# Optimization experiments

Hardware: AMD Instinct MI355X
Metric: run time of the kernel (lower is better)

The kernel has to match this reference:

```python
import jax, jax.numpy as jnp
import numpy as np

N = 50000   # nodes
E = 800000  # edges
D = 128     # input_dim == hidden_dim
R = 8       # num_relations
B = 2       # num_blocks


def setup_inputs() -> dict:
    key = jax.random.key(0)
    ks = jax.random.split(key, 9)
    x = jax.random.normal(ks[0], (N, D), dtype=jnp.float32)
    edge_index = jax.random.randint(ks[1], (2, E), 0, N, dtype=jnp.int32)
    edge_type = jax.random.randint(ks[2], (E,), 0, R, dtype=jnp.int32)
    s_blk = 1.0 / np.sqrt(D // B)
    s_root = 1.0 / np.sqrt(D)
    W1 = jax.random.normal(ks[3], (R, B, D // B, D // B), dtype=jnp.float32) * s_blk
    root1 = jax.random.normal(ks[4], (D, D), dtype=jnp.float32) * s_root
    b1 = jnp.zeros((D,), dtype=jnp.float32)
    W2 = jax.random.normal(ks[5], (R, B, D // B, D // B), dtype=jnp.float32) * s_blk
    root2 = jax.random.normal(ks[6], (D, D), dtype=jnp.float32) * s_root
    b2 = jnp.zeros((D,), dtype=jnp.float32)
    return {"x": x, "edge_index": edge_index, "edge_type": edge_type,
            "W1": W1, "root1": root1, "b1": b1,
            "W2": W2, "root2": root2, "b2": b2}


def rgcn_conv(x, src, dst, etype, W, root, bias):
    # PyG RGCNConv (num_blocks mode): per-relation MEAN aggregation of source
    # features, block-diagonal transform, summed over relations, plus root + bias.
    # Transform is linear, so aggregate first (saves per-edge matmuls).
    n = x.shape[0]
    r, b, ib, ob = W.shape
    xs = x[src]                                   # [E, d_in] gather
    seg = dst * r + etype                          # fused (node, relation) id
    sums = jax.ops.segment_sum(xs, seg, num_segments=n * r)        # [n*r, d_in]
    cnt = jax.ops.segment_sum(jnp.ones((xs.shape[0],), xs.dtype), seg,
                              num_segments=n * r)                   # [n*r]
    mean = sums / jnp.maximum(cnt, 1.0)[:, None]   # zero where no edges
    agg = mean.reshape(n, r, b, ib)                # [n, R, blocks, in/blocks]
    out = jnp.einsum('nrbc,rbcd->nbd', agg, W).reshape(n, b * ob)
    return out + x @ root + bias


def reference(x, edge_index, edge_type, W1, root1, b1, W2, root2, b2):
    src, dst = edge_index[0], edge_index[1]
    h = jax.nn.relu(rgcn_conv(x, src, dst, edge_type, W1, root1, b1))
    # dropout(p=0.2) is identity in eval mode (reference uses eval semantics)
    return rgcn_conv(h, src, dst, edge_type, W2, root2, b2)
```

## Files before the change

### kernel.cpp

```cpp
#include <hip/hip_runtime.h>

#define NN 50000
#define EE 800000
#define DD 128
#define RR 8
#define CELLS (NN * RR)
#define TILE_N 64
#define NBLK ((NN + TILE_N - 1) / TILE_N)
#define SCAN_CHUNK 1024
#define SCAN_BLOCKS ((CELLS + SCAN_CHUNK - 1) / SCAN_CHUNK)

typedef __attribute__((ext_vector_type(4))) float f32x4;
typedef __attribute__((ext_vector_type(8))) short s16x8;
union ABu { uint4 q; s16x8 v; };


__device__ __forceinline__ unsigned int packbf2(float a, float b) {
    unsigned int ua = __float_as_uint(a);
    unsigned int ub = __float_as_uint(b);
    ua = (ua + 0x7fffu + ((ua >> 16) & 1u)) >> 16;
    ub = (ub + 0x7fffu + ((ub >> 16) & 1u)) & 0xffff0000u;
    return ua | ub;
}

__device__ __forceinline__ void upadd16(float* sA, uint4 a, uint4 b) {
    unsigned int u[8] = {a.x, a.y, a.z, a.w, b.x, b.y, b.z, b.w};
#pragma unroll
    for (int j = 0; j < 8; ++j) {
        sA[2 * j]     += __uint_as_float(u[j] << 16);
        sA[2 * j + 1] += __uint_as_float(u[j] & 0xffff0000u);
    }
}

#define NB_A ((NN * 32 + 255) / 256)
#define NB_B 128
#define NB_C 32
#define NB_D ((EE + 255) / 256)

__global__ void prep_fused(const float* __restrict__ x, unsigned int* __restrict__ xb,
                           const float* __restrict__ W1, const float* __restrict__ W2,
                           unsigned int* __restrict__ Wb1, unsigned int* __restrict__ Wb2,
                           const float* __restrict__ r1, const float* __restrict__ r2,
                           unsigned int* __restrict__ rb1, unsigned int* __restrict__ rb2,
                           const int* __restrict__ dst, const int* __restrict__ et,
                           int* __restrict__ cnt) {
    int bid = blockIdx.x, tid = threadIdx.x;
    if (bid < NB_A) {
        int i = bid * 256 + tid;
        if (i < NN * 32) {
            float4 v = ((const float4*)x)[i];
            ((uint2*)xb)[i] = make_uint2(packbf2(v.x, v.y), packbf2(v.z, v.w));
        }
    } else if (bid < NB_A + NB_B) {
        int i = (bid - NB_A) * 256 + tid;
        int kp = i & 31, n = (i >> 5) & 63, rb = i >> 11;
        int s0 = (rb * 64 + 2 * kp) * 64 + n;
        int s1 = (rb * 64 + 2 * kp + 1) * 64 + n;
        Wb1[((rb * 64 + n) * 32) + kp] = packbf2(W1[s0], W1[s1]);
        Wb2[((rb * 64 + n) * 32) + kp] = packbf2(W2[s0], W2[s1]);
    } else if (bid < NB_A + NB_B + NB_C) {
        int i = (bid - NB_A - NB_B) * 256 + tid;
        int kp = i & 63, n = i >> 6;
        int s0 = (2 * kp) * 128 + n, s1 = (2 * kp + 1) * 128 + n;
        rb1[n * 64 + kp] = packbf2(r1[s0], r1[s1]);
        rb2[n * 64 + kp] = packbf2(r2[s0], r2[s1]);
    } else {
        int e = (bid - NB_A - NB_B - NB_C) * 256 + tid;
        if (e < EE) atomicAdd(&cnt[et[e] * NN + dst[e]], 1);
    }
}


__global__ __launch_bounds__(256) void scan1(const int* __restrict__ cnt,
                                             int* __restrict__ off, int* __restrict__ bsum) {
    __shared__ int s[256];
    int tid = threadIdx.x;
    int base = blockIdx.x * SCAN_CHUNK + tid * 4;
    int v[4];
#pragma unroll
    for (int i = 0; i < 4; ++i) v[i] = (base + i < CELLS) ? cnt[base + i] : 0;
    int tot = v[0] + v[1] + v[2] + v[3];
    s[tid] = tot;
    __syncthreads();
    for (int d = 1; d < 256; d <<= 1) {
        int t = (tid >= d) ? s[tid - d] : 0;
        __syncthreads();
        s[tid] += t;
        __syncthreads();
    }
    int excl = s[tid] - tot;
    if (tid == 255) bsum[blockIdx.x] = s[255];
    int run = excl;
#pragma unroll
    for (int i = 0; i < 4; ++i) {
        if (base + i < CELLS) off[base + i] = run;
        run += v[i];
    }
}

__global__ __launch_bounds__(256) void scan3(int* __restrict__ off, const int* __restrict__ bsum,
                                             int* __restrict__ cur) {
    __shared__ int red[256];
    int tid = threadIdx.x, bid = blockIdx.x;
    int a = 0;
    for (int i = tid; i < bid; i += 256) a += bsum[i];
    red[tid] = a;
    __syncthreads();
#pragma unroll
    for (int d = 128; d > 0; d >>= 1) {
        if (tid < d) red[tid] += red[tid + d];
        __syncthreads();
    }
    int add = red[0];
    int base = bid * SCAN_CHUNK + tid * 4;
#pragma unroll
    for (int i = 0; i < 4; ++i) {
        int c = base + i;
        if (c < CELLS) {
            int o = off[c] + add;
            off[c] = o;
            cur[c] = o;
        }
    }
    if (bid == 0 && tid == 0) off[CELLS] = EE;
}

__global__ void cell_scatter(const int* __restrict__ src, const int* __restrict__ dst,
                             const int* __restrict__ et, int* __restrict__ cur,
                             int* __restrict__ esrc) {
    int e = blockIdx.x * blockDim.x + threadIdx.x;
    if (e < EE) {
        int cell = et[e] * NN + dst[e];
        int pos = atomicAdd(&cur[cell], 1);
        esrc[pos] = src[e];
    }
}

template <int RELU, int WRITEF, int WRITEB>
__global__ __launch_bounds__(512, 4) void layer_fused(
    const unsigned int* __restrict__ xgb, const int* __restrict__ esrc,
    const int* __restrict__ off,
    const unsigned int* __restrict__ Wb, const unsigned int* __restrict__ rootb,
    const float* __restrict__ bias, float* __restrict__ outf,
    unsigned int* __restrict__ outb) {

    __shared__ unsigned int SH[8320];
    unsigned int* MT = SH;

    int tid = threadIdx.x;
    int n0 = blockIdx.x * TILE_N;
    int e = tid & 63, q = tid >> 6;
    int w = tid >> 6, l = tid & 63;
    int quad = l >> 4, li = l & 15;
    int b = w >> 2;

    f32x4 acc[4];
    {
        float bb = bias[16 * w + li];
#pragma unroll
        for (int mt = 0; mt < 4; ++mt) {
            acc[mt][0] = bb; acc[mt][1] = bb; acc[mt][2] = bb; acc[mt][3] = bb;
        }
    }

    int node = n0 + e;

    for (int r = 0; r < RR; ++r) {
        float sA[16];
#pragma unroll
        for (int i = 0; i < 16; ++i) sA[i] = 0.f;
        int ne = 0;
        if (node < NN) {
            int cell = r * NN + node;
            int o = off[cell];
            ne = off[cell + 1] - o;
            int t2 = 0;
            for (; t2 + 2 <= ne; t2 += 2) {
                int s0 = esrc[o + t2], s1 = esrc[o + t2 + 1];
                const uint4* p0 = (const uint4*)(xgb + (size_t)s0 * 64 + q * 8);
                const uint4* p1 = (const uint4*)(xgb + (size_t)s1 * 64 + q * 8);
                uint4 A0 = p0[0], A1 = p0[1];
                uint4 B0 = p1[0], B1 = p1[1];
                upadd16(sA, A0, A1);
                upadd16(sA, B0, B1);
            }
            if (t2 < ne) {
                int s0 = esrc[o + t2];
                const uint4* p0 = (const uint4*)(xgb + (size_t)s0 * 64 + q * 8);
                uint4 A0 = p0[0], A1 = p0[1];
                upadd16(sA, A0, A1);
            }
        }
        float sc = 1.0f / (float)max(ne, 1);

        __syncthreads();
#pragma unroll
        for (int i = 0; i < 8; ++i)
            MT[(8 * q + i) * 67 + e] = packbf2(sA[2 * i] * sc, sA[2 * i + 1] * sc);
        __syncthreads();

        const uint4* WbB = (const uint4*)(Wb + (((size_t)r * 2 + b) * 64) * 32);
        int nloc = (w & 3) * 16 + li;
#pragma unroll
        for (int kc = 0; kc < 2; ++kc) {
            ABu bf;
            bf.q = WbB[nloc * 8 + 4 * kc + quad];
#pragma unroll
            for (int mt = 0; mt < 4; ++mt) {
                ABu af;
                int base = (32 * b + 16 * kc + 4 * quad) * 67 + 16 * mt + li;
                af.q.x = MT[base]; af.q.y = MT[base + 67];
                af.q.z = MT[base + 134]; af.q.w = MT[base + 201];
                acc[mt] = __builtin_amdgcn_mfma_f32_16x16x32_bf16(af.v, bf.v, acc[mt], 0, 0, 0);
            }
        }
    }
    __syncthreads();

    if (node < NN) {
        const uint4* xr = (const uint4*)(xgb + (size_t)node * 64 + q * 8);
        uint4 X0 = xr[0], X1 = xr[1];
        MT[(8 * q + 0) * 67 + e] = X0.x;
        MT[(8 * q + 1) * 67 + e] = X0.y;
        MT[(8 * q + 2) * 67 + e] = X0.z;
        MT[(8 * q + 3) * 67 + e] = X0.w;
        MT[(8 * q + 4) * 67 + e] = X1.x;
        MT[(8 * q + 5) * 67 + e] = X1.y;
        MT[(8 * q + 6) * 67 + e] = X1.z;
        MT[(8 * q + 7) * 67 + e] = X1.w;
    } else {
#pragma unroll
        for (int i = 0; i < 8; ++i) MT[(8 * q + i) * 67 + e] = 0u;
    }
    __syncthreads();

    const uint4* RbB = (const uint4*)rootb;
#pragma unroll
    for (int kc = 0; kc < 4; ++kc) {
        ABu bf;
        bf.q = RbB[(16 * w + li) * 16 + 4 * kc + quad];
#pragma unroll
        for (int mt = 0; mt < 4; ++mt) {
            ABu af;
            int base = (16 * kc + 4 * quad) * 67 + 16 * mt + li;
            af.q.x = MT[base]; af.q.y = MT[base + 67];
            af.q.z = MT[base + 134]; af.q.w = MT[base + 201];
            acc[mt] = __builtin_amdgcn_mfma_f32_16x16x32_bf16(af.v, bf.v, acc[mt], 0, 0, 0);
        }
    }
    __syncthreads();

    float* OF = (float*)SH;
#pragma unroll
    for (int mt = 0; mt < 4; ++mt)
#pragma unroll
        for (int reg = 0; reg < 4; ++reg)
            OF[(16 * mt + 4 * quad + reg) * 130 + 16 * w + li] = acc[mt][reg];
    __syncthreads();

    if (WRITEB) {
        int p = tid & 63, rg = tid >> 6;
#pragma unroll 4
        for (int it = 0; it < 8; ++it) {
            int ee = it * 8 + rg, row = n0 + ee;
            if (row < NN) {
                float v0 = OF[ee * 130 + 2 * p], v1 = OF[ee * 130 + 2 * p + 1];
                if (RELU) { v0 = fmaxf(v0, 0.f); v1 = fmaxf(v1, 0.f); }
                outb[(size_t)row * 64 + p] = packbf2(v0, v1);
            }
        }
    }
    if (WRITEF) {
        int d4 = (tid & 31) * 4, rg = tid >> 5;
#pragma unroll 4
        for (int it = 0; it < 4; ++it) {
            int ee = it * 16 + rg, row = n0 + ee;
            if (row < NN) {
                float4 v = make_float4(OF[ee * 130 + d4], OF[ee * 130 + d4 + 1],
                                       OF[ee * 130 + d4 + 2], OF[ee * 130 + d4 + 3]);
                if (RELU) {
                    v.x = fmaxf(v.x, 0.f); v.y = fmaxf(v.y, 0.f);
                    v.z = fmaxf(v.z, 0.f); v.w = fmaxf(v.w, 0.f);
                }
                *(float4*)(outf + (size_t)row * DD + d4) = v;
            }
        }
    }
}


extern "C" void kernel_launch(void* const* d_in, const int* in_sizes, int n_in,
                              void* d_out, int out_size, void* d_ws, size_t ws_size,
                              hipStream_t stream) {
    const float* x     = (const float*)d_in[0];
    const int*   ei    = (const int*)d_in[1];
    const int*   src   = ei;
    const int*   dstp  = ei + EE;
    const int*   et    = (const int*)d_in[2];
    const float* W1    = (const float*)d_in[3];
    const float* root1 = (const float*)d_in[4];
    const float* b1    = (const float*)d_in[5];
    const float* W2    = (const float*)d_in[6];
    const float* root2 = (const float*)d_in[7];
    const float* b2    = (const float*)d_in[8];
    float* out = (float*)d_out;

    unsigned int* xb  = (unsigned int*)d_ws;
    unsigned int* hb  = xb + (size_t)NN * 64;
    int* cnt  = (int*)(hb + (size_t)NN * 64);
    int* off  = cnt + CELLS;
    int* cur  = off + CELLS + 1;
    int* bsum = cur + CELLS;
    int* esrc = bsum + 512;
    unsigned int* Wb1 = (unsigned int*)(esrc + EE);
    unsigned int* Wb2 = Wb1 + 32768;
    unsigned int* rb1 = Wb2 + 32768;
    unsigned int* rb2 = rb1 + 8192;

    hipMemsetAsync(cnt, 0, CELLS * sizeof(int), stream);
    prep_fused<<<NB_A + NB_B + NB_C + NB_D, 256, 0, stream>>>(
        x, xb, W1, W2, Wb1, Wb2, root1, root2, rb1, rb2, dstp, et, cnt);
    scan1<<<SCAN_BLOCKS, 256, 0, stream>>>(cnt, off, bsum);
    scan3<<<SCAN_BLOCKS, 256, 0, stream>>>(off, bsum, cur);
    cell_scatter<<<(EE + 255) / 256, 256, 0, stream>>>(src, dstp, et, cur, esrc);

    layer_fused<1, 0, 1><<<NBLK, 512, 0, stream>>>(xb, esrc, off, Wb1, rb1, b1,
                                                   nullptr, hb);
    layer_fused<0, 1, 0><<<NBLK, 512, 0, stream>>>(hb, esrc, off, Wb2, rb2, b2,
                                                   out, nullptr);
}
```

Baseline: 366.5 us.

## Double-buffer relation tiles and overlap gathers with previous relation's MFMA

The layer kernel now preloads all per-relation offsets, issues the first four edge gathers for relation r before running the MFMA for relation r-1, and writes the aggregated means into alternating shared-memory buffers. This allows one barrier per relation instead of two. The goal is to hide gather latency behind matrix work and cut synchronisation. The prep kernel also remaps its weight-packing indices so reads from the source weights are coalesced. In exchange, register pressure rises from the prefetched uint4s and LDS use grows slightly, which may affect occupancy.

```diff
diff --git a/kernel.cpp b/kernel.cpp
--- a/kernel.cpp
+++ b/kernel.cpp
@@ -53,14 +53,14 @@
         }
     } else if (bid < NB_A + NB_B) {
         int i = (bid - NB_A) * 256 + tid;
-        int kp = i & 31, n = (i >> 5) & 63, rb = i >> 11;
+        int n = i & 63, kp = (i >> 6) & 31, rb = i >> 11;
         int s0 = (rb * 64 + 2 * kp) * 64 + n;
         int s1 = (rb * 64 + 2 * kp + 1) * 64 + n;
         Wb1[((rb * 64 + n) * 32) + kp] = packbf2(W1[s0], W1[s1]);
         Wb2[((rb * 64 + n) * 32) + kp] = packbf2(W2[s0], W2[s1]);
     } else if (bid < NB_A + NB_B + NB_C) {
         int i = (bid - NB_A - NB_B) * 256 + tid;
-        int kp = i & 63, n = i >> 6;
+        int n = i & 127, kp = i >> 7;
         int s0 = (2 * kp) * 128 + n, s1 = (2 * kp + 1) * 128 + n;
         rb1[n * 64 + kp] = packbf2(r1[s0], r1[s1]);
         rb2[n * 64 + kp] = packbf2(r2[s0], r2[s1]);
@@ -136,6 +136,8 @@
     }
 }
 
+#define MTSZ 4288
+
 template <int RELU, int WRITEF, int WRITEB>
 __global__ __launch_bounds__(512, 4) void layer_fused(
     const unsigned int* __restrict__ xgb, const int* __restrict__ esrc,
@@ -144,15 +146,15 @@
     const float* __restrict__ bias, float* __restrict__ outf,
     unsigned int* __restrict__ outb) {
 
-    __shared__ unsigned int SH[8320];
-    unsigned int* MT = SH;
+    __shared__ unsigned int SH[2 * MTSZ];
 
     int tid = threadIdx.x;
     int n0 = blockIdx.x * TILE_N;
     int e = tid & 63, q = tid >> 6;
-    int w = tid >> 6, l = tid & 63;
+    int w = q, l = e;
     int quad = l >> 4, li = l & 15;
     int b = w >> 2;
+    int nloc = (w & 3) * 16 + li;
 
     f32x4 acc[4];
     {
@@ -165,72 +167,93 @@
 
     int node = n0 + e;
 
+    int ov[RR], nv[RR];
+#pragma unroll
     for (int r = 0; r < RR; ++r) {
+        if (node < NN) {
+            int c = r * NN + node;
+            int o = off[c];
+            ov[r] = o;
+            nv[r] = off[c + 1] - o;
+        } else { ov[r] = 0; nv[r] = 0; }
+    }
+
+#define MFMA_BLOCK(MTbase, rr) do {                                                   \
+    const uint4* WbB = (const uint4*)(Wb + (((size_t)(rr) * 2 + b) * 64) * 32);       \
+    _Pragma("unroll") for (int kc = 0; kc < 2; ++kc) {                                \
+        ABu bf; bf.q = WbB[nloc * 8 + 4 * kc + quad];                                 \
+        _Pragma("unroll") for (int mt = 0; mt < 4; ++mt) {                            \
+            ABu af; int base_ = (32 * b + 16 * kc + 4 * quad) * 67 + 16 * mt + li;    \
+            af.q.x = (MTbase)[base_];       af.q.y = (MTbase)[base_ + 67];            \
+            af.q.z = (MTbase)[base_ + 134]; af.q.w = (MTbase)[base_ + 201];           \
+            acc[mt] = __builtin_amdgcn_mfma_f32_16x16x32_bf16(af.v, bf.v, acc[mt], 0, 0, 0); \
+        } } } while (0)
+
+#pragma unroll
+    for (int r = 0; r < RR; ++r) {
+        int ne = nv[r], o = ov[r];
+        int s0 = 0, s1 = 0, s2 = 0, s3 = 0;
+        uint4 A0, B0, A1, B1, A2, B2, A3, B3;
+        if (ne > 0) s0 = esrc[o];
+        if (ne > 1) s1 = esrc[o + 1];
+        if (ne > 2) s2 = esrc[o + 2];
+        if (ne > 3) s3 = esrc[o + 3];
+        if (ne > 0) { const uint4* p = (const uint4*)(xgb + (size_t)s0 * 64 + q * 8); A0 = p[0]; B0 = p[1]; }
+        if (ne > 1) { const uint4* p = (const uint4*)(xgb + (size_t)s1 * 64 + q * 8); A1 = p[0]; B1 = p[1]; }
+        if (ne > 2) { const uint4* p = (const uint4*)(xgb + (size_t)s2 * 64 + q * 8); A2 = p[0]; B2 = p[1]; }
+        if (ne > 3) { const uint4* p = (const uint4*)(xgb + (size_t)s3 * 64 + q * 8); A3 = p[0]; B3 = p[1]; }
+
+        if (r > 0) MFMA_BLOCK(SH + ((r - 1) & 1) * MTSZ, r - 1);
+
         float sA[16];
 #pragma unroll
         for (int i = 0; i < 16; ++i) sA[i] = 0.f;
-        int ne = 0;
-        if (node < NN) {
-            int cell = r * NN + node;
-            int o = off[cell];
-            ne = off[cell + 1] - o;
-            int t2 = 0;
+        if (ne > 0) upadd16(sA, A0, B0);
+        if (ne > 1) upadd16(sA, A1, B1);
+        if (ne > 2) upadd16(sA, A2, B2);
+        if (ne > 3) upadd16(sA, A3, B3);
+        if (ne > 4) {
+            int t2 = 4;
             for (; t2 + 2 <= ne; t2 += 2) {
-                int s0 = esrc[o + t2], s1 = esrc[o + t2 + 1];
-                const uint4* p0 = (const uint4*)(xgb + (size_t)s0 * 64 + q * 8);
-                const uint4* p1 = (const uint4*)(xgb + (size_t)s1 * 64 + q * 8);
-                uint4 A0 = p0[0], A1 = p0[1];
-                uint4 B0 = p1[0], B1 = p1[1];
-                upadd16(sA, A0, A1);
-                upadd16(sA, B0, B1);
+                int u0 = esrc[o + t2], u1 = esrc[o + t2 + 1];
+                const uint4* p0 = (const uint4*)(xgb + (size_t)u0 * 64 + q * 8);
+                const uint4* p1 = (const uint4*)(xgb + (size_t)u1 * 64 + q * 8);
+                uint4 X0 = p0[0], X1 = p0[1];
+                uint4 Y0 = p1[0], Y1 = p1[1];
+                upadd16(sA, X0, X1);
+                upadd16(sA, Y0, Y1);
             }
             if (t2 < ne) {
-                int s0 = esrc[o + t2];
-                const uint4* p0 = (const uint4*)(xgb + (size_t)s0 * 64 + q * 8);
-                uint4 A0 = p0[0], A1 = p0[1];
-                upadd16(sA, A0, A1);
+                int u0 = esrc[o + t2];
+                const uint4* p0 = (const uint4*)(xgb + (size_t)u0 * 64 + q * 8);
+                uint4 X0 = p0[0], X1 = p0[1];
+                upadd16(sA, X0, X1);
             }
         }
         float sc = 1.0f / (float)max(ne, 1);
-
+        unsigned int* MTW = SH + (r & 1) * MTSZ;
+#pragma unroll
+        for (int i = 0; i < 8; ++i)
+            MTW[(8 * q + i) * 67 + e] = packbf2(sA[2 * i] * sc, sA[2 * i + 1] * sc);
         __syncthreads();
-#pragma unroll
-        for (int i = 0; i < 8; ++i)
-            MT[(8 * q + i) * 67 + e] = packbf2(sA[2 * i] * sc, sA[2 * i + 1] * sc);
-        __syncthreads();
-
-        const uint4* WbB = (const uint4*)(Wb + (((size_t)r * 2 + b) * 64) * 32);
-        int nloc = (w & 3) * 16 + li;
-#pragma unroll
-        for (int kc = 0; kc < 2; ++kc) {
-            ABu bf;
-            bf.q = WbB[nloc * 8 + 4 * kc + quad];
-#pragma unroll
-            for (int mt = 0; mt < 4; ++mt) {
-                ABu af;
-                int base = (32 * b + 16 * kc + 4 * quad) * 67 + 16 * mt + li;
-                af.q.x = MT[base]; af.q.y = MT[base + 67];
-                af.q.z = MT[base + 134]; af.q.w = MT[base + 201];
-                acc[mt] = __builtin_amdgcn_mfma_f32_16x16x32_bf16(af.v, bf.v, acc[mt], 0, 0, 0);
-            }
-        }
-    }
-    __syncthreads();
+    }
+
+    MFMA_BLOCK(SH + MTSZ, RR - 1);
 
     if (node < NN) {
         const uint4* xr = (const uint4*)(xgb + (size_t)node * 64 + q * 8);
         uint4 X0 = xr[0], X1 = xr[1];
-        MT[(8 * q + 0) * 67 + e] = X0.x;
-        MT[(8 * q + 1) * 67 + e] = X0.y;
-        MT[(8 * q + 2) * 67 + e] = X0.z;
-        MT[(8 * q + 3) * 67 + e] = X0.w;
-        MT[(8 * q + 4) * 67 + e] = X1.x;
-        MT[(8 * q + 5) * 67 + e] = X1.y;
-        MT[(8 * q + 6) * 67 + e] = X1.z;
-        MT[(8 * q + 7) * 67 + e] = X1.w;
+        SH[(8 * q + 0) * 67 + e] = X0.x;
+        SH[(8 * q + 1) * 67 + e] = X0.y;
+        SH[(8 * q + 2) * 67 + e] = X0.z;
+        SH[(8 * q + 3) * 67 + e] = X0.w;
+        SH[(8 * q + 4) * 67 + e] = X1.x;
+        SH[(8 * q + 5) * 67 + e] = X1.y;
+        SH[(8 * q + 6) * 67 + e] = X1.z;
+        SH[(8 * q + 7) * 67 + e] = X1.w;
     } else {
 #pragma unroll
-        for (int i = 0; i < 8; ++i) MT[(8 * q + i) * 67 + e] = 0u;
+        for (int i = 0; i < 8; ++i) SH[(8 * q + i) * 67 + e] = 0u;
     }
     __syncthreads();
 
@@ -243,8 +266,8 @@
         for (int mt = 0; mt < 4; ++mt) {
             ABu af;
             int base = (16 * kc + 4 * quad) * 67 + 16 * mt + li;
-            af.q.x = MT[base]; af.q.y = MT[base + 67];
-            af.q.z = MT[base + 134]; af.q.w = MT[base + 201];
+            af.q.x = SH[base]; af.q.y = SH[base + 67];
+            af.q.z = SH[base + 134]; af.q.w = SH[base + 201];
             acc[mt] = __builtin_amdgcn_mfma_f32_16x16x32_bf16(af.v, bf.v, acc[mt], 0, 0, 0);
         }
     }
@@ -286,6 +309,7 @@
             }
         }
     }
+#undef MFMA_BLOCK
 }
 
 
```

Measured after the change: 402.6 us. 9.8% more time.

## Aggregate neighbor features via one-hot MFMA over coalesced per-tile edge chunks

Applied to the files above, without the earlier changes.

Replaces the per-node serial gather-and-accumulate loop with a tile-level scheme. For each relation, the tile's contiguous edge range is processed in 64-edge chunks: rows are gathered coalesced into LDS, a one-hot selection matrix (built from the destination index packed into the low 6 bits of esrc) is written, and the segment sum is done with bf16 MFMA. This targets the load imbalance and poor coalescing of per-thread edge loops. In exchange it adds LDS use, extra syncs per chunk, and rounding of the one-hot product to bf16. It also relies on src<<6 fitting in 32 bits. The prep kernel's weight-packing loops are reindexed so global reads coalesce.

```diff
diff --git a/kernel.cpp b/kernel.cpp
--- a/kernel.cpp
+++ b/kernel.cpp
@@ -21,15 +21,6 @@
     ua = (ua + 0x7fffu + ((ua >> 16) & 1u)) >> 16;
     ub = (ub + 0x7fffu + ((ub >> 16) & 1u)) & 0xffff0000u;
     return ua | ub;
-}
-
-__device__ __forceinline__ void upadd16(float* sA, uint4 a, uint4 b) {
-    unsigned int u[8] = {a.x, a.y, a.z, a.w, b.x, b.y, b.z, b.w};
-#pragma unroll
-    for (int j = 0; j < 8; ++j) {
-        sA[2 * j]     += __uint_as_float(u[j] << 16);
-        sA[2 * j + 1] += __uint_as_float(u[j] & 0xffff0000u);
-    }
 }
 
 #define NB_A ((NN * 32 + 255) / 256)
@@ -53,14 +44,14 @@
         }
     } else if (bid < NB_A + NB_B) {
         int i = (bid - NB_A) * 256 + tid;
-        int kp = i & 31, n = (i >> 5) & 63, rb = i >> 11;
+        int n = i & 63, kp = (i >> 6) & 31, rb = i >> 11;
         int s0 = (rb * 64 + 2 * kp) * 64 + n;
         int s1 = (rb * 64 + 2 * kp + 1) * 64 + n;
         Wb1[((rb * 64 + n) * 32) + kp] = packbf2(W1[s0], W1[s1]);
         Wb2[((rb * 64 + n) * 32) + kp] = packbf2(W2[s0], W2[s1]);
     } else if (bid < NB_A + NB_B + NB_C) {
         int i = (bid - NB_A - NB_B) * 256 + tid;
-        int kp = i & 63, n = i >> 6;
+        int n = i & 127, kp = i >> 7;
         int s0 = (2 * kp) * 128 + n, s1 = (2 * kp + 1) * 128 + n;
         rb1[n * 64 + kp] = packbf2(r1[s0], r1[s1]);
         rb2[n * 64 + kp] = packbf2(r2[s0], r2[s1]);
@@ -130,29 +121,34 @@
                              int* __restrict__ esrc) {
     int e = blockIdx.x * blockDim.x + threadIdx.x;
     if (e < EE) {
-        int cell = et[e] * NN + dst[e];
+        int d = dst[e];
+        int cell = et[e] * NN + d;
         int pos = atomicAdd(&cur[cell], 1);
-        esrc[pos] = src[e];
+        esrc[pos] = (int)(((unsigned int)src[e] << 6) | (unsigned int)(d & 63));
     }
 }
 
 template <int RELU, int WRITEF, int WRITEB>
 __global__ __launch_bounds__(512, 4) void layer_fused(
-    const unsigned int* __restrict__ xgb, const int* __restrict__ esrc,
+    const unsigned int* __restrict__ xgb, const unsigned int* __restrict__ epk,
     const int* __restrict__ off,
     const unsigned int* __restrict__ Wb, const unsigned int* __restrict__ rootb,
     const float* __restrict__ bias, float* __restrict__ outf,
     unsigned int* __restrict__ outb) {
 
-    __shared__ unsigned int SH[8320];
-    unsigned int* MT = SH;
+    __shared__ __align__(16) unsigned int SH[11136];
+    unsigned int* GB  = SH;
+    unsigned int* SS  = SH + 4224;
+    unsigned int* MTp = SH + 6336;
+    float*        CF  = (float*)(SH + 10624);
 
     int tid = threadIdx.x;
     int n0 = blockIdx.x * TILE_N;
-    int e = tid & 63, q = tid >> 6;
     int w = tid >> 6, l = tid & 63;
     int quad = l >> 4, li = l & 15;
     int b = w >> 2;
+    int nloc = (w & 3) * 16 + li;
+    int node = n0 + l;
 
     f32x4 acc[4];
     {
@@ -163,44 +159,105 @@
         }
     }
 
-    int node = n0 + e;
+    int rng = 0;
+    {
+        int nend = n0 + TILE_N; if (nend > NN) nend = NN;
+        if (l < 8)       rng = off[l * NN + n0];
+        else if (l < 16) rng = off[(l - 8) * NN + nend];
+    }
+
+    uint4 z4 = make_uint4(0u, 0u, 0u, 0u);
+    ((uint4*)GB)[tid] = z4;
+    ((uint4*)GB)[512 + tid] = z4;
+    if (tid < 32) ((uint4*)GB)[1024 + tid] = z4;
+
+    if (w == 0) {
+        for (int r = 0; r < RR; ++r) {
+            float sc = 1.0f;
+            if (node < NN) {
+                int c = r * NN + node;
+                int ct = off[c + 1] - off[c];
+                sc = 1.0f / (float)max(ct, 1);
+            }
+            CF[r * 64 + l] = sc;
+        }
+    }
+    __syncthreads();
 
     for (int r = 0; r < RR; ++r) {
-        float sA[16];
-#pragma unroll
-        for (int i = 0; i < 16; ++i) sA[i] = 0.f;
-        int ne = 0;
-        if (node < NN) {
-            int cell = r * NN + node;
-            int o = off[cell];
-            ne = off[cell + 1] - o;
-            int t2 = 0;
-            for (; t2 + 2 <= ne; t2 += 2) {
-                int s0 = esrc[o + t2], s1 = esrc[o + t2 + 1];
-                const uint4* p0 = (const uint4*)(xgb + (size_t)s0 * 64 + q * 8);
-                const uint4* p1 = (const uint4*)(xgb + (size_t)s1 * 64 + q * 8);
-                uint4 A0 = p0[0], A1 = p0[1];
-                uint4 B0 = p1[0], B1 = p1[1];
-                upadd16(sA, A0, A1);
-                upadd16(sA, B0, B1);
-            }
-            if (t2 < ne) {
-                int s0 = esrc[o + t2];
-                const uint4* p0 = (const uint4*)(xgb + (size_t)s0 * 64 + q * 8);
-                uint4 A0 = p0[0], A1 = p0[1];
-                upadd16(sA, A0, A1);
-            }
-        }
-        float sc = 1.0f / (float)max(ne, 1);
-
+        int obeg = __shfl(rng, r);
+        int oend = __shfl(rng, 8 + r);
+        int nch = (oend - obeg + 63) >> 6;
+        if (nch == 0) continue;
+
+        f32x4 accS[4];
+#pragma unroll
+        for (int mt = 0; mt < 4; ++mt) {
+            accS[mt][0] = 0.f; accS[mt][1] = 0.f; accS[mt][2] = 0.f; accS[mt][3] = 0.f;
+        }
+
+        for (int ch = 0; ch < nch; ++ch) {
+            int t0 = obeg + ch * 64;
+            int m = oend - t0; if (m > 64) m = 64;
+            if (ch > 0) __syncthreads();
+
+            int sbase = (4 * w) * 66;
+#pragma unroll
+            for (int k = 0; k < 4; ++k) SS[sbase + k * 64 + l] = 0u;
+            if (l < 8) SS[sbase + 256 + l] = 0u;
+
+            unsigned int rec = 0u;
+            if (l < 8 && 8 * w + l < m) {
+                rec = epk[t0 + 8 * w + l];
+                ((unsigned short*)SS)[((4 * w + (l >> 1)) * 66 + (rec & 63u)) * 2 + (l & 1)] = 0x3F80u;
+            }
+
+            unsigned int uu[8];
+#pragma unroll
+            for (int j = 0; j < 8; ++j) {
+                unsigned int rj = __shfl(rec, j);
+                uu[j] = (8 * w + j < m) ? xgb[(rj & 0xffffffc0u) + (unsigned)l] : 0u;
+            }
+            unsigned short* GUS = (unsigned short*)GB;
+#pragma unroll
+            for (int j = 0; j < 8; ++j) {
+                int e = 8 * w + j;
+                if (e < m) {
+                    GUS[((2 * l) * 33 + (e >> 1)) * 2 + (e & 1)]     = (unsigned short)(uu[j] & 0xffffu);
+                    GUS[((2 * l + 1) * 33 + (e >> 1)) * 2 + (e & 1)] = (unsigned short)(uu[j] >> 16);
+                }
+            }
+            __syncthreads();
+
+#pragma unroll
+            for (int kc = 0; kc < 2; ++kc) {
+                ABu bf;
+                int gb = (16 * w + li) * 33 + 16 * kc + 4 * quad;
+                bf.q.x = GB[gb]; bf.q.y = GB[gb + 1]; bf.q.z = GB[gb + 2]; bf.q.w = GB[gb + 3];
+#pragma unroll
+                for (int mt = 0; mt < 4; ++mt) {
+                    ABu af;
+                    int sb = (16 * kc + 4 * quad) * 66 + 16 * mt + li;
+                    af.q.x = SS[sb]; af.q.y = SS[sb + 66]; af.q.z = SS[sb + 132]; af.q.w = SS[sb + 198];
+                    accS[mt] = __builtin_amdgcn_mfma_f32_16x16x32_bf16(af.v, bf.v, accS[mt], 0, 0, 0);
+                }
+            }
+        }
+
+#pragma unroll
+        for (int mt = 0; mt < 4; ++mt) {
+#pragma unroll
+            for (int j = 0; j < 4; ++j) {
+                int nd = 16 * mt + 4 * quad + j;
+                float v = accS[mt][j] * CF[r * 64 + nd];
+                float vp = __shfl_xor(v, 1);
+                if (!(li & 1))
+                    MTp[(8 * w + (li >> 1)) * 67 + nd] = packbf2(v, vp);
+            }
+        }
         __syncthreads();
-#pragma unroll
-        for (int i = 0; i < 8; ++i)
-            MT[(8 * q + i) * 67 + e] = packbf2(sA[2 * i] * sc, sA[2 * i + 1] * sc);
-        __syncthreads();
 
         const uint4* WbB = (const uint4*)(Wb + (((size_t)r * 2 + b) * 64) * 32);
-        int nloc = (w & 3) * 16 + li;
 #pragma unroll
         for (int kc = 0; kc < 2; ++kc) {
             ABu bf;
@@ -208,9 +265,9 @@
 #pragma unroll
             for (int mt = 0; mt < 4; ++mt) {
                 ABu af;
-                int base = (32 * b + 16 * kc + 4 * quad) * 67 + 16 * mt + li;
-                af.q.x = MT[base]; af.q.y = MT[base + 67];
-                af.q.z = MT[base + 134]; af.q.w = MT[base + 201];
+                int base_ = (32 * b + 16 * kc + 4 * quad) * 67 + 16 * mt + li;
+                af.q.x = MTp[base_]; af.q.y = MTp[base_ + 67];
+                af.q.z = MTp[base_ + 134]; af.q.w = MTp[base_ + 201];
                 acc[mt] = __builtin_amdgcn_mfma_f32_16x16x32_bf16(af.v, bf.v, acc[mt], 0, 0, 0);
             }
         }
@@ -218,19 +275,19 @@
     __syncthreads();
 
     if (node < NN) {
-        const uint4* xr = (const uint4*)(xgb + (size_t)node * 64 + q * 8);
+        const uint4* xr = (const uint4*)(xgb + (size_t)node * 64 + w * 8);
         uint4 X0 = xr[0], X1 = xr[1];
-        MT[(8 * q + 0) * 67 + e] = X0.x;
-        MT[(8 * q + 1) * 67 + e] = X0.y;
-        MT[(8 * q + 2) * 67 + e] = X0.z;
-        MT[(8 * q + 3) * 67 + e] = X0.w;
-        MT[(8 * q + 4) * 67 + e] = X1.x;
-        MT[(8 * q + 5) * 67 + e] = X1.y;
-        MT[(8 * q + 6) * 67 + e] = X1.z;
-        MT[(8 * q + 7) * 67 + e] = X1.w;
+        MTp[(8 * w + 0) * 67 + l] = X0.x;
+        MTp[(8 * w + 1) * 67 + l] = X0.y;
+        MTp[(8 * w + 2) * 67 + l] = X0.z;
+        MTp[(8 * w + 3) * 67 + l] = X0.w;
+        MTp[(8 * w + 4) * 67 + l] = X1.x;
+        MTp[(8 * w + 5) * 67 + l] = X1.y;
+        MTp[(8 * w + 6) * 67 + l] = X1.z;
+        MTp[(8 * w + 7) * 67 + l] = X1.w;
     } else {
 #pragma unroll
-        for (int i = 0; i < 8; ++i) MT[(8 * q + i) * 67 + e] = 0u;
+        for (int i = 0; i < 8; ++i) MTp[(8 * w + i) * 67 + l] = 0u;
     }
     __syncthreads();
 
@@ -243,8 +300,8 @@
         for (int mt = 0; mt < 4; ++mt) {
             ABu af;
             int base = (16 * kc + 4 * quad) * 67 + 16 * mt + li;
-            af.q.x = MT[base]; af.q.y = MT[base + 67];
-            af.q.z = MT[base + 134]; af.q.w = MT[base + 201];
+            af.q.x = MTp[base]; af.q.y = MTp[base + 67];
+            af.q.z = MTp[base + 134]; af.q.w = MTp[base + 201];
             acc[mt] = __builtin_amdgcn_mfma_f32_16x16x32_bf16(af.v, bf.v, acc[mt], 0, 0, 0);
         }
     }
@@ -324,8 +381,8 @@
     scan3<<<SCAN_BLOCKS, 256, 0, stream>>>(off, bsum, cur);
     cell_scatter<<<(EE + 255) / 256, 256, 0, stream>>>(src, dstp, et, cur, esrc);
 
-    layer_fused<1, 0, 1><<<NBLK, 512, 0, stream>>>(xb, esrc, off, Wb1, rb1, b1,
-                                                   nullptr, hb);
-    layer_fused<0, 1, 0><<<NBLK, 512, 0, stream>>>(hb, esrc, off, Wb2, rb2, b2,
-                                                   out, nullptr);
-}
+    layer_fused<1, 0, 1><<<NBLK, 512, 0, stream>>>(xb, (const unsigned int*)esrc, off,
+                                                   Wb1, rb1, b1, nullptr, hb);
+    layer_fused<0, 1, 0><<<NBLK, 512, 0, stream>>>(hb, (const unsigned int*)esrc, off,
+                                                   Wb2, rb2, b2, out, nullptr);
+}
```

After: 480.6 us. +31.1%, slower.

## Stage tile's contiguous edge-source rows cooperatively into LDS for relation aggregation

Applied to the files above, without the earlier changes.

Since edges are sorted by (relation, node) cell, a tile of 64 nodes has one contiguous edge range per relation. The aggregation now loads that range in chunks of 128 rows: each wave gathers whole 256-byte bf16 rows into shared memory with coalesced per-lane 4-byte loads, and each thread then sums its own node's slice from LDS. Before, every thread issued its own scattered 16-byte gathers. The change also precomputes the per-relation offsets in registers and reorders the weight-packing index math so global reads coalesce. It adds extra barriers and LDS traffic, and all 512 threads now wait on the busiest node in each chunk.

```diff
diff --git a/kernel.cpp b/kernel.cpp
--- a/kernel.cpp
+++ b/kernel.cpp
@@ -21,15 +21,6 @@
     ua = (ua + 0x7fffu + ((ua >> 16) & 1u)) >> 16;
     ub = (ub + 0x7fffu + ((ub >> 16) & 1u)) & 0xffff0000u;
     return ua | ub;
-}
-
-__device__ __forceinline__ void upadd16(float* sA, uint4 a, uint4 b) {
-    unsigned int u[8] = {a.x, a.y, a.z, a.w, b.x, b.y, b.z, b.w};
-#pragma unroll
-    for (int j = 0; j < 8; ++j) {
-        sA[2 * j]     += __uint_as_float(u[j] << 16);
-        sA[2 * j + 1] += __uint_as_float(u[j] & 0xffff0000u);
-    }
 }
 
 #define NB_A ((NN * 32 + 255) / 256)
@@ -53,14 +44,14 @@
         }
     } else if (bid < NB_A + NB_B) {
         int i = (bid - NB_A) * 256 + tid;
-        int kp = i & 31, n = (i >> 5) & 63, rb = i >> 11;
+        int n = i & 63, kp = (i >> 6) & 31, rb = i >> 11;
         int s0 = (rb * 64 + 2 * kp) * 64 + n;
         int s1 = (rb * 64 + 2 * kp + 1) * 64 + n;
         Wb1[((rb * 64 + n) * 32) + kp] = packbf2(W1[s0], W1[s1]);
         Wb2[((rb * 64 + n) * 32) + kp] = packbf2(W2[s0], W2[s1]);
     } else if (bid < NB_A + NB_B + NB_C) {
         int i = (bid - NB_A - NB_B) * 256 + tid;
-        int kp = i & 63, n = i >> 6;
+        int n = i & 127, kp = i >> 7;
         int s0 = (2 * kp) * 128 + n, s1 = (2 * kp + 1) * 128 + n;
         rb1[n * 64 + kp] = packbf2(r1[s0], r1[s1]);
         rb2[n * 64 + kp] = packbf2(r2[s0], r2[s1]);
@@ -136,6 +127,7 @@
     }
 }
 
+
 template <int RELU, int WRITEF, int WRITEB>
 __global__ __launch_bounds__(512, 4) void layer_fused(
     const unsigned int* __restrict__ xgb, const int* __restrict__ esrc,
@@ -144,15 +136,17 @@
     const float* __restrict__ bias, float* __restrict__ outf,
     unsigned int* __restrict__ outb) {
 
-    __shared__ unsigned int SH[8320];
-    unsigned int* MT = SH;
+    __shared__ unsigned int SH[8320 + 4288];
+    unsigned int* G  = SH;
+    unsigned int* MT = SH + 8320;
 
     int tid = threadIdx.x;
     int n0 = blockIdx.x * TILE_N;
     int e = tid & 63, q = tid >> 6;
-    int w = tid >> 6, l = tid & 63;
+    int w = q, l = e;
     int quad = l >> 4, li = l & 15;
     int b = w >> 2;
+    int nloc = (w & 3) * 16 + li;
 
     f32x4 acc[4];
     {
@@ -165,55 +159,84 @@
 
     int node = n0 + e;
 
+    int ov[RR], nv[RR];
+#pragma unroll
     for (int r = 0; r < RR; ++r) {
+        if (node < NN) {
+            int c = r * NN + node;
+            int o = off[c];
+            ov[r] = o;
+            nv[r] = off[c + 1] - o;
+        } else { ov[r] = 0; nv[r] = 0; }
+    }
+
+    int rng = 0;
+    {
+        int nend = n0 + TILE_N; if (nend > NN) nend = NN;
+        if (l < 8)       rng = off[l * NN + n0];
+        else if (l < 16) rng = off[(l - 8) * NN + nend];
+    }
+
+#define MFMA_BLOCK(rr) do {                                                           \
+    const uint4* WbB = (const uint4*)(Wb + (((size_t)(rr) * 2 + b) * 64) * 32);       \
+    _Pragma("unroll") for (int kc = 0; kc < 2; ++kc) {                                \
+        ABu bf; bf.q = WbB[nloc * 8 + 4 * kc + quad];                                 \
+        _Pragma("unroll") for (int mt = 0; mt < 4; ++mt) {                            \
+            ABu af; int base_ = (32 * b + 16 * kc + 4 * quad) * 67 + 16 * mt + li;    \
+            af.q.x = MT[base_];       af.q.y = MT[base_ + 67];                        \
+            af.q.z = MT[base_ + 134]; af.q.w = MT[base_ + 201];                       \
+            acc[mt] = __builtin_amdgcn_mfma_f32_16x16x32_bf16(af.v, bf.v, acc[mt], 0, 0, 0); \
+        } } } while (0)
+
+#pragma unroll
+    for (int r = 0; r < RR; ++r) {
+        int obeg = __shfl(rng, r);
+        int oend = __shfl(rng, 8 + r);
+        int a0 = ov[r];
+        int b0 = a0 + nv[r];
+
         float sA[16];
 #pragma unroll
         for (int i = 0; i < 16; ++i) sA[i] = 0.f;
-        int ne = 0;
-        if (node < NN) {
-            int cell = r * NN + node;
-            int o = off[cell];
-            ne = off[cell + 1] - o;
-            int t2 = 0;
-            for (; t2 + 2 <= ne; t2 += 2) {
-                int s0 = esrc[o + t2], s1 = esrc[o + t2 + 1];
-                const uint4* p0 = (const uint4*)(xgb + (size_t)s0 * 64 + q * 8);
-                const uint4* p1 = (const uint4*)(xgb + (size_t)s1 * 64 + q * 8);
-                uint4 A0 = p0[0], A1 = p0[1];
-                uint4 B0 = p1[0], B1 = p1[1];
-                upadd16(sA, A0, A1);
-                upadd16(sA, B0, B1);
-            }
-            if (t2 < ne) {
-                int s0 = esrc[o + t2];
-                const uint4* p0 = (const uint4*)(xgb + (size_t)s0 * 64 + q * 8);
-                uint4 A0 = p0[0], A1 = p0[1];
-                upadd16(sA, A0, A1);
-            }
-        }
-        float sc = 1.0f / (float)max(ne, 1);
-
+
+        for (int c0 = obeg; c0 < oend; c0 += 128) {
+            int m = oend - c0; if (m > 128) m = 128;
+            __syncthreads();
+
+            int idx = 0;
+            if (l < 16) {
+                int j = w * 16 + l;
+                if (j < m) idx = esrc[c0 + j];
+            }
+#pragma unroll
+            for (int k = 0; k < 16; ++k) {
+                int j = w * 16 + k;
+                int rj = __shfl(idx, k);
+                if (j < m) G[j * 65 + l] = xgb[(size_t)rj * 64 + l];
+            }
+            __syncthreads();
+
+            int lo = a0 > c0 ? a0 : c0;
+            int c1 = c0 + m;
+            int hi = b0 < c1 ? b0 : c1;
+            for (int t = lo; t < hi; ++t) {
+                int gb = (t - c0) * 65 + 8 * q;
+#pragma unroll
+                for (int i = 0; i < 8; ++i) {
+                    unsigned int u = G[gb + i];
+                    sA[2 * i]     += __uint_as_float(u << 16);
+                    sA[2 * i + 1] += __uint_as_float(u & 0xffff0000u);
+                }
+            }
+        }
+
+        float sc = 1.0f / (float)max(nv[r], 1);
         __syncthreads();
 #pragma unroll
         for (int i = 0; i < 8; ++i)
             MT[(8 * q + i) * 67 + e] = packbf2(sA[2 * i] * sc, sA[2 * i + 1] * sc);
         __syncthreads();
-
-        const uint4* WbB = (const uint4*)(Wb + (((size_t)r * 2 + b) * 64) * 32);
-        int nloc = (w & 3) * 16 + li;
-#pragma unroll
-        for (int kc = 0; kc < 2; ++kc) {
-            ABu bf;
-            bf.q = WbB[nloc * 8 + 4 * kc + quad];
-#pragma unroll
-            for (int mt = 0; mt < 4; ++mt) {
-                ABu af;
-                int base = (32 * b + 16 * kc + 4 * quad) * 67 + 16 * mt + li;
-                af.q.x = MT[base]; af.q.y = MT[base + 67];
-                af.q.z = MT[base + 134]; af.q.w = MT[base + 201];
-                acc[mt] = __builtin_amdgcn_mfma_f32_16x16x32_bf16(af.v, bf.v, acc[mt], 0, 0, 0);
-            }
-        }
+        MFMA_BLOCK(r);
     }
     __syncthreads();
 
@@ -286,6 +309,7 @@
             }
         }
     }
+#undef MFMA_BLOCK
 }
 
 
```

New measurement: 527.1 us. +43.8%, slower.
